# Optimization experiments

Hardware: AMD Instinct MI355X
Metric: run time of the kernel (lower is better)

## Reference

```python
import jax, jax.numpy as jnp
import numpy as np

H = 1024
NS, NQ, S = 32, 64, 256
ADAPT_STEPS = 5


def _mlp_ln(x, W1, b1, W2, b2, g, be):
    # Linear -> ReLU -> Linear -> LayerNorm (dropout is identity in eval)
    h = jax.nn.relu(x @ W1 + b1) @ W2 + b2
    mu = h.mean(-1, keepdims=True)
    var = ((h - mu) ** 2).mean(-1, keepdims=True)
    return g * (h - mu) / jnp.sqrt(var + 1e-5) + be


def setup_inputs() -> dict:
    key = jax.random.key(0)
    ks = jax.random.split(key, 16)
    d = {}
    d['support_embeddings'] = jax.random.normal(ks[0], (NS, S, H), jnp.float32)
    d['query_embeddings'] = jax.random.normal(ks[1], (NQ, S, H), jnp.float32)
    d['support_labels'] = jax.random.randint(ks[2], (NS, S), 0, 3)
    w = lambda k, fi, fo: jax.random.normal(k, (fi, fo), jnp.float32) * (1.0 / np.sqrt(fi))
    # aspect_aware encoder
    d['aw_W1'] = w(ks[3], H, H); d['aw_b1'] = jnp.zeros((H,), jnp.float32)
    d['aw_W2'] = w(ks[4], H, H); d['aw_b2'] = jnp.zeros((H,), jnp.float32)
    d['aw_g'] = jnp.ones((H,), jnp.float32); d['aw_be'] = jnp.zeros((H,), jnp.float32)
    # aspect_contrastive encoder
    d['ct_W1'] = w(ks[5], H, H); d['ct_b1'] = jnp.zeros((H,), jnp.float32)
    d['ct_W2'] = w(ks[6], H, H); d['ct_b2'] = jnp.zeros((H,), jnp.float32)
    d['ct_g'] = jnp.ones((H,), jnp.float32); d['ct_be'] = jnp.zeros((H,), jnp.float32)
    # adaptation net (randomly-initialized 2-layer MLP in the torch code)
    d['ad_W1'] = w(ks[7], H, H); d['ad_b1'] = jnp.zeros((H,), jnp.float32)
    d['ad_W2'] = w(ks[8], H, H); d['ad_b2'] = jnp.zeros((H,), jnp.float32)
    # meta classifier
    d['cl_W1'] = w(ks[9], 2 * H, H); d['cl_b1'] = jnp.zeros((H,), jnp.float32)
    d['cl_W2'] = w(ks[10], H, 64); d['cl_b2'] = jnp.zeros((64,), jnp.float32)
    d['cl_W3'] = w(ks[11], 64, 3); d['cl_b3'] = jnp.zeros((3,), jnp.float32)
    return d


def reference(support_embeddings, query_embeddings, support_labels,
              aw_W1, aw_b1, aw_W2, aw_b2, aw_g, aw_be,
              ct_W1, ct_b1, ct_W2, ct_b2, ct_g, ct_be,
              ad_W1, ad_b1, ad_W2, ad_b2,
              cl_W1, cl_b1, cl_W2, cl_b2, cl_W3, cl_b3):
    # --- encode support set, build per-sentence aspect prototypes ---
    aw_s = _mlp_ln(support_embeddings, aw_W1, aw_b1, aw_W2, aw_b2, aw_g, aw_be)  # [NS,S,H]
    mask = (support_labels > 0).astype(aw_s.dtype)[..., None]                    # [NS,S,1]
    cnt = jnp.maximum(mask.sum(axis=1), 1.0)                                     # [NS,1]
    protos = (aw_s * mask).sum(axis=1) / cnt                                     # [NS,H] masked mean
    pn = protos / jnp.maximum(jnp.linalg.norm(protos, axis=-1, keepdims=True), 1e-8)

    # --- meta-adaptation: fused over all (query, token) pairs, 5 steps ---
    adapted = query_embeddings
    for _ in range(ADAPT_STEPS):
        qn = adapted / jnp.maximum(jnp.linalg.norm(adapted, axis=-1, keepdims=True), 1e-8)
        sims = jnp.einsum('qsh,ph->qsp', qn, pn)           # cosine similarities
        wts = jax.nn.softmax(sims, axis=-1)
        infl = jnp.einsum('qsp,ph->qsh', wts, protos)      # prototype influence
        adapted = jax.nn.relu((adapted + infl) @ ad_W1 + ad_b1) @ ad_W2 + ad_b2

    # --- classify adapted query tokens ---
    q_aw = _mlp_ln(adapted, aw_W1, aw_b1, aw_W2, aw_b2, aw_g, aw_be)
    q_ct = _mlp_ln(adapted, ct_W1, ct_b1, ct_W2, ct_b2, ct_g, ct_be)
    comb = jnp.concatenate([q_aw, q_ct], axis=-1)          # [NQ,S,2H]
    h = jax.nn.relu(comb @ cl_W1 + cl_b1)
    h = jax.nn.relu(h @ cl_W2 + cl_b2)
    preds = h @ cl_W3 + cl_b3                              # [NQ,S,3]
    return preds
```

## Files before the change

### kernel.cpp

```cpp
#include <hip/hip_runtime.h>
#include <hip/hip_bf16.h>

#define H 1024
#define NS 32
#define SS 256
#define T_Q 16384
#define M_S 8192

typedef __hip_bfloat16 bf16;
typedef short short8 __attribute__((ext_vector_type(8)));
typedef float floatx4 __attribute__((ext_vector_type(4)));

__device__ __forceinline__ float ldf(const bf16& v) { return __bfloat162float(v); }

__device__ __forceinline__ void split2(float v, bf16& h, bf16& l) {
  h = __float2bfloat16(v);
  l = __float2bfloat16(v - __bfloat162float(h));
}

__device__ __forceinline__ void gl2lds16(const void* g, void* l) {
  __builtin_amdgcn_global_load_lds(
      (const __attribute__((address_space(1))) unsigned int*)g,
      (__attribute__((address_space(3))) unsigned int*)l, 16, 0, 0);
}

__device__ __forceinline__ short8 ld8s(const bf16* p) { return *(const short8*)p; }

__global__ __launch_bounds__(256) void conv_split(const float* __restrict__ in,
                                                  bf16* __restrict__ oh,
                                                  bf16* __restrict__ ol, int n)
{
  int i = blockIdx.x * 256 + threadIdx.x;
  if (i < n) { bf16 h, l; split2(in[i], h, l); oh[i] = h; ol[i] = l; }
}

__global__ __launch_bounds__(256) void transpose_split(
    const float* __restrict__ W, bf16* __restrict__ Wh, bf16* __restrict__ Wl,
    int K, int N)
{
  __shared__ float t[32][33];
  int n0 = blockIdx.x * 32, k0 = blockIdx.y * 32;
  int tx = threadIdx.x & 31, ty = threadIdx.x >> 5;
#pragma unroll
  for (int i = 0; i < 32; i += 8)
    t[ty + i][tx] = W[(size_t)(k0 + ty + i) * N + (n0 + tx)];
  __syncthreads();
#pragma unroll
  for (int i = 0; i < 32; i += 8) {
    bf16 h, l; split2(t[tx][ty + i], h, l);
    size_t o = (size_t)(n0 + ty + i) * K + (k0 + tx);
    Wh[o] = h;
    if (Wl) Wl[o] = l;
  }
}

template<bool RELU, bool HASWL>
__global__ __launch_bounds__(512) void gemm3p(
    const bf16* __restrict__ A0h, const bf16* __restrict__ A0l,
    const bf16* __restrict__ A1h, const bf16* __restrict__ A1l,
    const bf16* __restrict__ Wh,  const bf16* __restrict__ Wl,
    const float* __restrict__ bias,
    bf16* __restrict__ Ch, bf16* __restrict__ Cl,
    int M, int N, int K0, int Ktot)
{
  (void)M;
  __shared__ __align__(16) bf16 lds[3 * 24576];
  const int tid = threadIdx.x;
  const int w = tid >> 6, l = tid & 63;
  const int bm0 = blockIdx.x * 256, bn0 = blockIdx.y * 128;
  const int wr = w >> 1, wn = w & 1;
  const int m16 = l & 15, quad = l >> 4;
  const int srow = l & 15;
  const int scol = (l >> 4) * 8;

  floatx4 acc[4][4];
#pragma unroll
  for (int i = 0; i < 4; i++)
#pragma unroll
    for (int j = 0; j < 4; j++) { acc[i][j][0]=0.f; acc[i][j][1]=0.f; acc[i][j][2]=0.f; acc[i][j][3]=0.f; }

  const size_t raA0 = (size_t)(bm0 + (2 * w)     * 16 + srow) * H + scol;
  const size_t raA1 = (size_t)(bm0 + (2 * w + 1) * 16 + srow) * H + scol;
  const size_t raB  = (size_t)(bn0 + w * 16 + srow) * Ktot + scol;
  const int nT = Ktot >> 5;

  auto stage = [&](int t) {
    const int k0 = t << 5;
    const bf16 *Abh, *Abl; int ke;
    if (k0 < K0) { Abh = A0h; Abl = A0l; ke = k0; }
    else         { Abh = A1h; Abl = A1l; ke = k0 - K0; }
    bf16* buf = lds + (t % 3) * 24576;
    gl2lds16(Abh + raA0 + ke, buf + (2 * w)     * 512);
    gl2lds16(Abh + raA1 + ke, buf + (2 * w + 1) * 512);
    gl2lds16(Abl + raA0 + ke, buf + 8192 + (2 * w)     * 512);
    gl2lds16(Abl + raA1 + ke, buf + 8192 + (2 * w + 1) * 512);
    gl2lds16(Wh + raB + k0, buf + 16384 + w * 512);
    if (HASWL) gl2lds16(Wl + raB + k0, buf + 20480 + w * 512);
  };

  stage(0);
  if (nT > 1) stage(1);

  const int la = l * 8;
  for (int t = 0; t < nT; ++t) {
    const bf16* buf = lds + (t % 3) * 24576;
    if (t + 2 < nT) {
      stage(t + 2);
      if (HASWL) asm volatile("s_waitcnt vmcnt(12)" ::: "memory");
      else       asm volatile("s_waitcnt vmcnt(10)" ::: "memory");
    } else if (t + 1 < nT) {
      if (HASWL) asm volatile("s_waitcnt vmcnt(6)" ::: "memory");
      else       asm volatile("s_waitcnt vmcnt(5)" ::: "memory");
    } else {
      asm volatile("s_waitcnt vmcnt(0)" ::: "memory");
    }
    __builtin_amdgcn_s_barrier();

    const bf16* bA  = buf + (wr * 4) * 512 + la;
    const bf16* bAl = bA + 8192;
    const bf16* bB  = buf + 16384 + (wn * 4) * 512 + la;
    const bf16* bBl = bB + 4096;

    short8 bh[4], bl8[4];
#pragma unroll
    for (int ni = 0; ni < 4; ni++) bh[ni] = ld8s(bB + ni * 512);
    if (HASWL) {
#pragma unroll
      for (int ni = 0; ni < 4; ni++) bl8[ni] = ld8s(bBl + ni * 512);
    }

#define MM3(MI, AH, AL)                                                                            \
    _Pragma("unroll")                                                                              \
    for (int ni = 0; ni < 4; ni++) {                                                               \
      acc[MI][ni] = __builtin_amdgcn_mfma_f32_16x16x32_bf16(AH, bh[ni],  acc[MI][ni], 0, 0, 0);    \
      acc[MI][ni] = __builtin_amdgcn_mfma_f32_16x16x32_bf16(AL, bh[ni],  acc[MI][ni], 0, 0, 0);    \
      if (HASWL)                                                                                   \
        acc[MI][ni] = __builtin_amdgcn_mfma_f32_16x16x32_bf16(AH, bl8[ni], acc[MI][ni], 0, 0, 0);  \
    }

    {
      short8 a0h = ld8s(bA),          a1h = ld8s(bA + 512);
      short8 a0l = ld8s(bAl),         a1l = ld8s(bAl + 512);
      __builtin_amdgcn_s_setprio(1);
      MM3(0, a0h, a0l)
      MM3(1, a1h, a1l)
      __builtin_amdgcn_s_setprio(0);
    }
    __builtin_amdgcn_s_barrier();
    {
      short8 a2h = ld8s(bA + 1024),   a3h = ld8s(bA + 1536);
      short8 a2l = ld8s(bAl + 1024),  a3l = ld8s(bAl + 1536);
      __builtin_amdgcn_s_setprio(1);
      MM3(2, a2h, a2l)
      MM3(3, a3h, a3l)
      __builtin_amdgcn_s_setprio(0);
    }
    __builtin_amdgcn_s_barrier();
#undef MM3
  }

#pragma unroll
  for (int mi = 0; mi < 4; mi++) {
#pragma unroll
    for (int ni = 0; ni < 4; ni++) {
      int row0 = bm0 + wr * 64 + mi * 16 + quad * 4;
      int col  = bn0 + wn * 64 + ni * 16 + m16;
      float bv = bias ? bias[col] : 0.f;
#pragma unroll
      for (int r = 0; r < 4; r++) {
        float v = acc[mi][ni][r] + bv;
        if (RELU) v = fmaxf(v, 0.f);
        bf16 h, lo; split2(v, h, lo);
        size_t o = (size_t)(row0 + r) * N + col;
        Ch[o] = h; Cl[o] = lo;
      }
    }
  }
}

__global__ __launch_bounds__(256) void ln_pair(
    bf16* __restrict__ hh, bf16* __restrict__ hl,
    const float* __restrict__ g, const float* __restrict__ be)
{
  int row = blockIdx.x;
  bf16* ph = hh + (size_t)row * H;
  bf16* pl = hl + (size_t)row * H;
  int tid = threadIdx.x;
  float v[4];
  float s = 0.f, sq = 0.f;
#pragma unroll
  for (int j = 0; j < 4; j++) {
    int hi = tid + 256 * j;
    v[j] = ldf(ph[hi]) + ldf(pl[hi]);
    s += v[j]; sq += v[j] * v[j];
  }
  __shared__ float rs[256], rq[256];
  rs[tid] = s; rq[tid] = sq; __syncthreads();
  for (int o = 128; o; o >>= 1) {
    if (tid < o) { rs[tid] += rs[tid + o]; rq[tid] += rq[tid + o]; }
    __syncthreads();
  }
  float mu   = rs[0] * (1.0f / H);
  float var  = rq[0] * (1.0f / H) - mu * mu;
  float rstd = rsqrtf(var + 1e-5f);
#pragma unroll
  for (int j = 0; j < 4; j++) {
    int hi = tid + 256 * j;
    bf16 h, l; split2(g[hi] * (v[j] - mu) * rstd + be[hi], h, l);
    ph[hi] = h; pl[hi] = l;
  }
}

__global__ __launch_bounds__(256) void proto_kernel(
    const bf16* __restrict__ eh, const bf16* __restrict__ el,
    const int* __restrict__ labels, float* __restrict__ protos_out)
{
  int p = blockIdx.x;
  int tid = threadIdx.x;
  __shared__ unsigned char lbl[SS];
  lbl[tid] = (labels[p * SS + tid] > 0) ? 1 : 0;
  __syncthreads();
  float acc[4] = {0.f, 0.f, 0.f, 0.f};
  int cnt = 0;
  const bf16* bh = eh + (size_t)p * SS * H;
  const bf16* bl = el + (size_t)p * SS * H;
  for (int s = 0; s < SS; s++) {
    if (lbl[s]) {
      cnt++;
      const bf16* rh = bh + (size_t)s * H;
      const bf16* rl = bl + (size_t)s * H;
#pragma unroll
      for (int j = 0; j < 4; j++)
        acc[j] += ldf(rh[tid + 256 * j]) + ldf(rl[tid + 256 * j]);
    }
  }
  float ic = 1.0f / fmaxf((float)cnt, 1.0f);
#pragma unroll
  for (int j = 0; j < 4; j++) protos_out[p * H + tid + 256 * j] = acc[j] * ic;
}

__global__ __launch_bounds__(256) void pn_kernel(
    const float* __restrict__ protos, bf16* __restrict__ pnh, bf16* __restrict__ pnl)
{
  int p = blockIdx.x;
  int tid = threadIdx.x;
  __shared__ float red[256];
  float v[4];
  float sq = 0.f;
#pragma unroll
  for (int j = 0; j < 4; j++) { v[j] = protos[p * H + tid + 256 * j]; sq += v[j] * v[j]; }
  red[tid] = sq; __syncthreads();
  for (int o = 128; o; o >>= 1) {
    if (tid < o) red[tid] += red[tid + o];
    __syncthreads();
  }
  float inv = 1.0f / fmaxf(sqrtf(red[0]), 1e-8f);
#pragma unroll
  for (int j = 0; j < 4; j++) {
    bf16 h, l; split2(v[j] * inv, h, l);
    pnh[p * H + tid + 256 * j] = h;
    pnl[p * H + tid + 256 * j] = l;
  }
}

__global__ __launch_bounds__(256) void rownorm_pair(
    const bf16* __restrict__ hh, const bf16* __restrict__ hl, float* __restrict__ rn)
{
  int row = blockIdx.x;
  int tid = threadIdx.x;
  const bf16* ph = hh + (size_t)row * H;
  const bf16* pl = hl + (size_t)row * H;
  float s = 0.f;
#pragma unroll
  for (int j = 0; j < 4; j++) {
    float v = ldf(ph[tid + 256 * j]) + ldf(pl[tid + 256 * j]);
    s += v * v;
  }
  __shared__ float rs[256];
  rs[tid] = s; __syncthreads();
  for (int o = 128; o; o >>= 1) {
    if (tid < o) rs[tid] += rs[tid + o];
    __syncthreads();
  }
  if (tid == 0) rn[row] = 1.0f / fmaxf(sqrtf(rs[0]), 1e-8f);
}

__global__ __launch_bounds__(256) void sims_mfma(
    const bf16* __restrict__ Ah, const bf16* __restrict__ Al,
    const bf16* __restrict__ Bh, const bf16* __restrict__ Bl,
    float* __restrict__ sims)
{
  __shared__ bf16 AsH[64 * 32];
  __shared__ bf16 AsL[64 * 32];
  __shared__ bf16 BsH[32 * 32];
  __shared__ bf16 BsL[32 * 32];
  const int tid = threadIdx.x;
  const int w = tid >> 6, l = tid & 63;
  const int bm0 = blockIdx.x * 64;
  const int m16 = l & 15, quad = l >> 4;
  const int sr = l >> 2;
  const int sc = (l & 3) * 8;

  floatx4 acc[2];
#pragma unroll
  for (int nt = 0; nt < 2; nt++) { acc[nt][0]=0.f; acc[nt][1]=0.f; acc[nt][2]=0.f; acc[nt][3]=0.f; }

  for (int k0 = 0; k0 < H; k0 += 32) {
    gl2lds16(Ah + (size_t)(bm0 + w * 16 + sr) * H + k0 + sc, &AsH[w * 512]);
    gl2lds16(Al + (size_t)(bm0 + w * 16 + sr) * H + k0 + sc, &AsL[w * 512]);
    if (w < 2) gl2lds16(Bh + (size_t)(w * 16 + sr) * H + k0 + sc, &BsH[w * 512]);
    else       gl2lds16(Bl + (size_t)((w - 2) * 16 + sr) * H + k0 + sc, &BsL[(w - 2) * 512]);
    __syncthreads();

    short8 ah  = *(const short8*)&AsH[(w * 16 + m16) * 32 + quad * 8];
    short8 al8 = *(const short8*)&AsL[(w * 16 + m16) * 32 + quad * 8];
#pragma unroll
    for (int nt = 0; nt < 2; nt++) {
      short8 bh  = *(const short8*)&BsH[(nt * 16 + m16) * 32 + quad * 8];
      short8 bl8 = *(const short8*)&BsL[(nt * 16 + m16) * 32 + quad * 8];
      acc[nt] = __builtin_amdgcn_mfma_f32_16x16x32_bf16(ah,  bh,  acc[nt], 0, 0, 0);
      acc[nt] = __builtin_amdgcn_mfma_f32_16x16x32_bf16(al8, bh,  acc[nt], 0, 0, 0);
      acc[nt] = __builtin_amdgcn_mfma_f32_16x16x32_bf16(ah,  bl8, acc[nt], 0, 0, 0);
    }
    __syncthreads();
  }

#pragma unroll
  for (int nt = 0; nt < 2; nt++) {
    int col  = nt * 16 + m16;
    int row0 = bm0 + w * 16 + quad * 4;
#pragma unroll
    for (int r = 0; r < 4; r++)
      sims[(size_t)(row0 + r) * 32 + col] = acc[nt][r];
  }
}

__global__ __launch_bounds__(256) void softmax32(
    const float* __restrict__ sims, const float* __restrict__ rn,
    float* __restrict__ wts)
{
  int t = blockIdx.x * 8 + (threadIdx.x >> 5);
  int p = threadIdx.x & 31;
  float s = sims[(size_t)t * 32 + p] * rn[t];
  float m = s;
#pragma unroll
  for (int o = 16; o; o >>= 1) m = fmaxf(m, __shfl_xor(m, o, 64));
  float e = __expf(s - m);
  float sum = e;
#pragma unroll
  for (int o = 16; o; o >>= 1) sum += __shfl_xor(sum, o, 64);
  wts[(size_t)t * 32 + p] = e / sum;
}

__global__ __launch_bounds__(256) void infl16(
    const bf16* __restrict__ ah, const bf16* __restrict__ al,
    const float* __restrict__ wts, const float* __restrict__ protos,
    bf16* __restrict__ oh, bf16* __restrict__ ol)
{
  int t0 = blockIdx.x * 16;
  int tid = threadIdx.x;
  __shared__ float wl[16][32];
  for (int i = tid; i < 512; i += 256)
    wl[i >> 5][i & 31] = wts[(size_t)(t0 + (i >> 5)) * 32 + (i & 31)];
  __syncthreads();
  int c0 = tid * 4;
  float acc[16][4];
#pragma unroll
  for (int tk = 0; tk < 16; tk++) {
    const bf16* rh = ah + (size_t)(t0 + tk) * H + c0;
    const bf16* rl = al + (size_t)(t0 + tk) * H + c0;
#pragma unroll
    for (int j = 0; j < 4; j++) acc[tk][j] = ldf(rh[j]) + ldf(rl[j]);
  }
  for (int p = 0; p < 32; p++) {
    float4 pv = *(const float4*)&protos[p * H + c0];
#pragma unroll
    for (int tk = 0; tk < 16; tk++) {
      float w = wl[tk][p];
      acc[tk][0] += w * pv.x; acc[tk][1] += w * pv.y;
      acc[tk][2] += w * pv.z; acc[tk][3] += w * pv.w;
    }
  }
#pragma unroll
  for (int tk = 0; tk < 16; tk++) {
    bf16* wh = oh + (size_t)(t0 + tk) * H + c0;
    bf16* wo = ol + (size_t)(t0 + tk) * H + c0;
#pragma unroll
    for (int j = 0; j < 4; j++) { bf16 h, lo; split2(acc[tk][j], h, lo); wh[j] = h; wo[j] = lo; }
  }
}

__global__ __launch_bounds__(256) void gemm_small(
    const bf16* __restrict__ Ah, const bf16* __restrict__ Al,
    const float* __restrict__ W, const float* __restrict__ bias,
    float* __restrict__ C, int M, int N, int K)
{
  const int BK = 16;
  __shared__ float As[BK][64];
  __shared__ float Bs[BK][64];
  int tid = threadIdx.x;
  int tx = tid & 15, ty = tid >> 4;
  int bn0 = blockIdx.x * 64;
  int bm0 = blockIdx.y * 64;
  float acc[4][4] = {};
  int am = tid >> 2, ak = (tid & 3) * 4;
  int bk = tid >> 4, bn = (tid & 15) * 4;
  const bf16* Aph = Ah + (size_t)(bm0 + am) * K + ak;
  const bf16* Apl = Al + (size_t)(bm0 + am) * K + ak;
  const float* Wptr = W + (size_t)bk * N + bn0 + bn;
  for (int k0 = 0; k0 < K; k0 += BK) {
#pragma unroll
    for (int c = 0; c < 4; c++) As[ak + c][am] = ldf(Aph[c]) + ldf(Apl[c]);
#pragma unroll
    for (int c = 0; c < 4; c++) Bs[bk][bn + c] = Wptr[c];
    __syncthreads();
#pragma unroll
    for (int k = 0; k < BK; k++) {
      float a[4], b[4];
#pragma unroll
      for (int i = 0; i < 4; i++) a[i] = As[k][ty * 4 + i];
#pragma unroll
      for (int j = 0; j < 4; j++) b[j] = Bs[k][tx * 4 + j];
#pragma unroll
      for (int i = 0; i < 4; i++)
#pragma unroll
        for (int j = 0; j < 4; j++)
          acc[i][j] += a[i] * b[j];
    }
    __syncthreads();
    Aph += BK; Apl += BK;
    Wptr += (size_t)BK * N;
  }
#pragma unroll
  for (int i = 0; i < 4; i++) {
    float* Crow = C + (size_t)(bm0 + ty * 4 + i) * N + bn0;
#pragma unroll
    for (int j = 0; j < 4; j++) {
      int n = tx * 4 + j;
      Crow[n] = fmaxf(acc[i][j] + bias[bn0 + n], 0.f);
    }
  }
}

__global__ __launch_bounds__(256) void FewShotABSALearner_46935402610855_kernel(
    const float* __restrict__ h2, const float* __restrict__ W3,
    const float* __restrict__ b3, float* __restrict__ out,
    int t0, int nElem, int out_size)
{
  int idx = blockIdx.x * 256 + threadIdx.x;
  if (idx >= nElem) return;
  int t = idx / 3, c = idx - t * 3;
  float acc = b3[c];
  const float* hr = h2 + (size_t)t * 64;
#pragma unroll
  for (int k = 0; k < 64; k++) acc += hr[k] * W3[k * 3 + c];
  int oi = t0 * 3 + idx;
  if (oi < out_size) out[oi] = acc;
}

extern "C" void kernel_launch(void* const* d_in, const int* in_sizes, int n_in,
                              void* d_out, int out_size, void* d_ws, size_t ws_size,
                              hipStream_t stream)
{
  (void)in_sizes; (void)n_in;
  const float* sup   = (const float*)d_in[0];
  const float* qry   = (const float*)d_in[1];
  const int*   lab   = (const int*)d_in[2];
  const float *aw_W1 = (const float*)d_in[3],  *aw_b1 = (const float*)d_in[4];
  const float *aw_W2 = (const float*)d_in[5],  *aw_b2 = (const float*)d_in[6];
  const float *aw_g  = (const float*)d_in[7],  *aw_be = (const float*)d_in[8];
  const float *ct_W1 = (const float*)d_in[9],  *ct_b1 = (const float*)d_in[10];
  const float *ct_W2 = (const float*)d_in[11], *ct_b2 = (const float*)d_in[12];
  const float *ct_g  = (const float*)d_in[13], *ct_be = (const float*)d_in[14];
  const float *ad_W1 = (const float*)d_in[15], *ad_b1 = (const float*)d_in[16];
  const float *ad_W2 = (const float*)d_in[17], *ad_b2 = (const float*)d_in[18];
  const float *cl_W1 = (const float*)d_in[19], *cl_b1 = (const float*)d_in[20];
  const float *cl_W2 = (const float*)d_in[21], *cl_b2 = (const float*)d_in[22];
  const float *cl_W3 = (const float*)d_in[23], *cl_b3 = (const float*)d_in[24];
  float* out = (float*)d_out;

  const size_t MB = 1 << 20;
  int C; bool clLo = true;
  if      (ws_size >= (size_t)239403008) C = 16384;
  else if (ws_size >= (size_t)136609792) C = 8192;
  else if (ws_size >= (size_t)85213184)  C = 4096;
  else if (ws_size >= (size_t)59514880)  C = 2048;
  else if (ws_size >= (size_t)46665728)  C = 1024;
  else { C = 1024; clLo = false; }
  const int Cs = (C < M_S) ? C : M_S;
  const size_t actB = (size_t)C * H * sizeof(bf16);

  char* ws = (char*)d_ws;
  size_t off = 0;
  auto nxt = [&](size_t b) { char* p = ws + off; off += b; return p; };
  bf16* sqw[12];
  for (int i = 0; i < 12; i++) sqw[i] = (bf16*)nxt(2 * MB);
  bf16 *aw1h = sqw[0], *aw1l = sqw[1], *aw2h = sqw[2],  *aw2l = sqw[3];
  bf16 *ct1h = sqw[4], *ct1l = sqw[5], *ct2h = sqw[6],  *ct2l = sqw[7];
  bf16 *ad1h = sqw[8], *ad1l = sqw[9], *ad2h = sqw[10], *ad2l = sqw[11];
  bf16* clW1h = (bf16*)nxt(4 * MB);
  bf16* clW1l = clLo ? (bf16*)nxt(4 * MB) : nullptr;
  float* protos = (float*)nxt(NS * H * 4);
  bf16*  pnh    = (bf16*)nxt(NS * H * 2);
  bf16*  pnl    = (bf16*)nxt(NS * H * 2);
  char*  ub     = nxt((size_t)C * 256);
  float* h2c   = (float*)ub;
  float* simsb = (float*)ub;
  float* wtsb  = (float*)(ub + (size_t)C * 128);
  float* rn    = (float*)nxt((size_t)C * 4);
  bf16 *R0h = (bf16*)nxt(actB), *R0l = (bf16*)nxt(actB);
  bf16 *R1h = (bf16*)nxt(actB), *R1l = (bf16*)nxt(actB);
  bf16 *R2h = (bf16*)nxt(actB), *R2l = (bf16*)nxt(actB);

  dim3 blk(256);
  dim3 blk2(512);
  dim3 tg(32, 32);
  dim3 gg2(C / 256, H / 128);
  dim3 gs2(Cs / 256, H / 128);

  transpose_split<<<tg, blk, 0, stream>>>(aw_W1, aw1h, aw1l, H, H);
  transpose_split<<<tg, blk, 0, stream>>>(aw_W2, aw2h, aw2l, H, H);
  transpose_split<<<tg, blk, 0, stream>>>(ct_W1, ct1h, ct1l, H, H);
  transpose_split<<<tg, blk, 0, stream>>>(ct_W2, ct2h, ct2l, H, H);
  transpose_split<<<tg, blk, 0, stream>>>(ad_W1, ad1h, ad1l, H, H);
  transpose_split<<<tg, blk, 0, stream>>>(ad_W2, ad2h, ad2l, H, H);
  transpose_split<<<dim3(32, 64), blk, 0, stream>>>(cl_W1, clW1h, clW1l, 2 * H, H);

  for (int sc = 0; sc < M_S / Cs; sc++) {
    conv_split<<<(Cs * H) / 256, blk, 0, stream>>>(sup + (size_t)sc * Cs * H, R0h, R0l, Cs * H);
    gemm3p<true , true><<<gs2, blk2, 0, stream>>>(R0h, R0l, R0h, R0l, aw1h, aw1l, aw_b1, R1h, R1l, Cs, H, H, H);
    gemm3p<false, true><<<gs2, blk2, 0, stream>>>(R1h, R1l, R1h, R1l, aw2h, aw2l, aw_b2, R2h, R2l, Cs, H, H, H);
    ln_pair<<<Cs, blk, 0, stream>>>(R2h, R2l, aw_g, aw_be);
    proto_kernel<<<Cs / SS, blk, 0, stream>>>(R2h, R2l, lab + sc * Cs,
                                              protos + (size_t)sc * (Cs / SS) * H);
  }
  pn_kernel<<<NS, blk, 0, stream>>>(protos, pnh, pnl);

  for (int qc = 0; qc < T_Q / C; qc++) {
    const float* q0 = qry + (size_t)qc * C * H;
    conv_split<<<(C * H) / 256, blk, 0, stream>>>(q0, R2h, R2l, C * H);
    for (int it = 0; it < 5; it++) {
      rownorm_pair<<<C, blk, 0, stream>>>(R2h, R2l, rn);
      sims_mfma<<<C / 64, blk, 0, stream>>>(R2h, R2l, pnh, pnl, simsb);
      softmax32<<<C / 8, blk, 0, stream>>>(simsb, rn, wtsb);
      infl16<<<C / 16, blk, 0, stream>>>(R2h, R2l, wtsb, protos, R0h, R0l);
      gemm3p<true , true><<<gg2, blk2, 0, stream>>>(R0h, R0l, R0h, R0l, ad1h, ad1l, ad_b1, R1h, R1l, C, H, H, H);
      gemm3p<false, true><<<gg2, blk2, 0, stream>>>(R1h, R1l, R1h, R1l, ad2h, ad2l, ad_b2, R2h, R2l, C, H, H, H);
    }
    gemm3p<true , true><<<gg2, blk2, 0, stream>>>(R2h, R2l, R2h, R2l, aw1h, aw1l, aw_b1, R0h, R0l, C, H, H, H);
    gemm3p<false, true><<<gg2, blk2, 0, stream>>>(R0h, R0l, R0h, R0l, aw2h, aw2l, aw_b2, R1h, R1l, C, H, H, H);
    ln_pair<<<C, blk, 0, stream>>>(R1h, R1l, aw_g, aw_be);
    gemm3p<true , true><<<gg2, blk2, 0, stream>>>(R2h, R2l, R2h, R2l, ct1h, ct1l, ct_b1, R0h, R0l, C, H, H, H);
    gemm3p<false, true><<<gg2, blk2, 0, stream>>>(R0h, R0l, R0h, R0l, ct2h, ct2l, ct_b2, R2h, R2l, C, H, H, H);
    ln_pair<<<C, blk, 0, stream>>>(R2h, R2l, ct_g, ct_be);
    if (clLo)
      gemm3p<true, true ><<<gg2, blk2, 0, stream>>>(R1h, R1l, R2h, R2l, clW1h, clW1l, cl_b1, R0h, R0l, C, H, H, 2 * H);
    else
      gemm3p<true, false><<<gg2, blk2, 0, stream>>>(R1h, R1l, R2h, R2l, clW1h, nullptr, cl_b1, R0h, R0l, C, H, H, 2 * H);
    gemm_small<<<dim3(1, C / 64), blk, 0, stream>>>(R0h, R0l, cl_W2, cl_b2, h2c, C, 64, H);
    FewShotABSALearner_46935402610855_kernel<<<(C * 3 + 255) / 256, blk, 0, stream>>>(
        h2c, cl_W3, cl_b3, out, qc * C, C * 3, out_size);
  }
}
```

Before: 2.740 ms.

## Enlarge GEMM tile to 256x256 with XCD-aware block mapping and double buffering

The split-bf16 GEMM now computes a 256x256 output tile per 512-thread block instead of 256x128. Each wave holds an 8x4 accumulator grid and A fragments are software-prefetched across the m-loop. The LDS pipeline drops from triple to double buffering, and the 2D grid becomes a 1D grid remapped so blocks on the same XCD share a B column tile. The intent is more arithmetic per loaded byte and better L2 locality. The cost is more accumulator registers, less prefetch depth and fewer blocks, which may hurt occupancy and latency hiding.

```diff
diff --git a/kernel.cpp b/kernel.cpp
--- a/kernel.cpp
+++ b/kernel.cpp
@@ -55,7 +55,7 @@
 }
 
 template<bool RELU, bool HASWL>
-__global__ __launch_bounds__(512) void gemm3p(
+__global__ __launch_bounds__(512, 2) void gemm3p(
     const bf16* __restrict__ A0h, const bf16* __restrict__ A0l,
     const bf16* __restrict__ A1h, const bf16* __restrict__ A1l,
     const bf16* __restrict__ Wh,  const bf16* __restrict__ Wl,
@@ -64,24 +64,30 @@
     int M, int N, int K0, int Ktot)
 {
   (void)M;
-  __shared__ __align__(16) bf16 lds[3 * 24576];
+  __shared__ __align__(16) bf16 lds[2 * 32768];
   const int tid = threadIdx.x;
   const int w = tid >> 6, l = tid & 63;
-  const int bm0 = blockIdx.x * 256, bn0 = blockIdx.y * 128;
-  const int wr = w >> 1, wn = w & 1;
+  const int nbm = gridDim.x >> 2;
+  const int lid = blockIdx.x;
+  const int xcd = lid & 7, ib = lid >> 3;
+  const int half = nbm >> 1;
+  const int bn = xcd >> 1;
+  const int bm = (xcd & 1) * half + ib;
+  const int wr = w >> 2, wn = w & 3;
   const int m16 = l & 15, quad = l >> 4;
   const int srow = l & 15;
   const int scol = (l >> 4) * 8;
 
-  floatx4 acc[4][4];
-#pragma unroll
-  for (int i = 0; i < 4; i++)
+  floatx4 acc[8][4];
+#pragma unroll
+  for (int i = 0; i < 8; i++)
 #pragma unroll
     for (int j = 0; j < 4; j++) { acc[i][j][0]=0.f; acc[i][j][1]=0.f; acc[i][j][2]=0.f; acc[i][j][3]=0.f; }
 
-  const size_t raA0 = (size_t)(bm0 + (2 * w)     * 16 + srow) * H + scol;
-  const size_t raA1 = (size_t)(bm0 + (2 * w + 1) * 16 + srow) * H + scol;
-  const size_t raB  = (size_t)(bn0 + w * 16 + srow) * Ktot + scol;
+  const size_t raA0 = (size_t)(bm * 256 + (2 * w)     * 16 + srow) * H + scol;
+  const size_t raA1 = (size_t)(bm * 256 + (2 * w + 1) * 16 + srow) * H + scol;
+  const size_t raB0 = (size_t)(bn * 256 + (2 * w)     * 16 + srow) * Ktot + scol;
+  const size_t raB1 = (size_t)(bn * 256 + (2 * w + 1) * 16 + srow) * Ktot + scol;
   const int nT = Ktot >> 5;
 
   auto stage = [&](int t) {
@@ -89,86 +95,75 @@
     const bf16 *Abh, *Abl; int ke;
     if (k0 < K0) { Abh = A0h; Abl = A0l; ke = k0; }
     else         { Abh = A1h; Abl = A1l; ke = k0 - K0; }
-    bf16* buf = lds + (t % 3) * 24576;
+    bf16* buf = lds + (t & 1) * 32768;
     gl2lds16(Abh + raA0 + ke, buf + (2 * w)     * 512);
     gl2lds16(Abh + raA1 + ke, buf + (2 * w + 1) * 512);
-    gl2lds16(Abl + raA0 + ke, buf + 8192 + (2 * w)     * 512);
-    gl2lds16(Abl + raA1 + ke, buf + 8192 + (2 * w + 1) * 512);
-    gl2lds16(Wh + raB + k0, buf + 16384 + w * 512);
-    if (HASWL) gl2lds16(Wl + raB + k0, buf + 20480 + w * 512);
+    gl2lds16(Abl + raA0 + ke, buf + 8192  + (2 * w)     * 512);
+    gl2lds16(Abl + raA1 + ke, buf + 8192  + (2 * w + 1) * 512);
+    gl2lds16(Wh + raB0 + k0, buf + 16384 + (2 * w)     * 512);
+    gl2lds16(Wh + raB1 + k0, buf + 16384 + (2 * w + 1) * 512);
+    if (HASWL) {
+      gl2lds16(Wl + raB0 + k0, buf + 24576 + (2 * w)     * 512);
+      gl2lds16(Wl + raB1 + k0, buf + 24576 + (2 * w + 1) * 512);
+    }
   };
 
   stage(0);
-  if (nT > 1) stage(1);
 
   const int la = l * 8;
   for (int t = 0; t < nT; ++t) {
-    const bf16* buf = lds + (t % 3) * 24576;
-    if (t + 2 < nT) {
-      stage(t + 2);
-      if (HASWL) asm volatile("s_waitcnt vmcnt(12)" ::: "memory");
-      else       asm volatile("s_waitcnt vmcnt(10)" ::: "memory");
-    } else if (t + 1 < nT) {
-      if (HASWL) asm volatile("s_waitcnt vmcnt(6)" ::: "memory");
-      else       asm volatile("s_waitcnt vmcnt(5)" ::: "memory");
+    const bf16* buf = lds + (t & 1) * 32768;
+    __builtin_amdgcn_s_barrier();
+    if (t + 1 < nT) {
+      stage(t + 1);
+      if (HASWL) asm volatile("s_waitcnt vmcnt(8)" ::: "memory");
+      else       asm volatile("s_waitcnt vmcnt(6)" ::: "memory");
     } else {
       asm volatile("s_waitcnt vmcnt(0)" ::: "memory");
     }
     __builtin_amdgcn_s_barrier();
 
-    const bf16* bA  = buf + (wr * 4) * 512 + la;
-    const bf16* bAl = bA + 8192;
-    const bf16* bB  = buf + 16384 + (wn * 4) * 512 + la;
-    const bf16* bBl = bB + 4096;
+    const bf16* pA  = buf + (wr * 8) * 512 + la;
+    const bf16* pAl = pA + 8192;
+    const bf16* pB  = buf + 16384 + (wn * 4) * 512 + la;
+    const bf16* pBl = pB + 8192;
 
     short8 bh[4], bl8[4];
 #pragma unroll
-    for (int ni = 0; ni < 4; ni++) bh[ni] = ld8s(bB + ni * 512);
+    for (int nt = 0; nt < 4; nt++) bh[nt] = ld8s(pB + nt * 512);
     if (HASWL) {
 #pragma unroll
-      for (int ni = 0; ni < 4; ni++) bl8[ni] = ld8s(bBl + ni * 512);
-    }
-
-#define MM3(MI, AH, AL)                                                                            \
-    _Pragma("unroll")                                                                              \
-    for (int ni = 0; ni < 4; ni++) {                                                               \
-      acc[MI][ni] = __builtin_amdgcn_mfma_f32_16x16x32_bf16(AH, bh[ni],  acc[MI][ni], 0, 0, 0);    \
-      acc[MI][ni] = __builtin_amdgcn_mfma_f32_16x16x32_bf16(AL, bh[ni],  acc[MI][ni], 0, 0, 0);    \
-      if (HASWL)                                                                                   \
-        acc[MI][ni] = __builtin_amdgcn_mfma_f32_16x16x32_bf16(AH, bl8[ni], acc[MI][ni], 0, 0, 0);  \
-    }
-
-    {
-      short8 a0h = ld8s(bA),          a1h = ld8s(bA + 512);
-      short8 a0l = ld8s(bAl),         a1l = ld8s(bAl + 512);
+      for (int nt = 0; nt < 4; nt++) bl8[nt] = ld8s(pBl + nt * 512);
+    }
+
+    short8 ah = ld8s(pA), al8 = ld8s(pAl);
+#pragma unroll
+    for (int mt = 0; mt < 8; mt++) {
+      short8 nh = ah, nl = al8;
+      if (mt < 7) { nh = ld8s(pA + (mt + 1) * 512); nl = ld8s(pAl + (mt + 1) * 512); }
       __builtin_amdgcn_s_setprio(1);
-      MM3(0, a0h, a0l)
-      MM3(1, a1h, a1l)
+#pragma unroll
+      for (int nt = 0; nt < 4; nt++) {
+        acc[mt][nt] = __builtin_amdgcn_mfma_f32_16x16x32_bf16(ah,  bh[nt],  acc[mt][nt], 0, 0, 0);
+        acc[mt][nt] = __builtin_amdgcn_mfma_f32_16x16x32_bf16(al8, bh[nt],  acc[mt][nt], 0, 0, 0);
+        if (HASWL)
+          acc[mt][nt] = __builtin_amdgcn_mfma_f32_16x16x32_bf16(ah, bl8[nt], acc[mt][nt], 0, 0, 0);
+      }
       __builtin_amdgcn_s_setprio(0);
-    }
-    __builtin_amdgcn_s_barrier();
-    {
-      short8 a2h = ld8s(bA + 1024),   a3h = ld8s(bA + 1536);
-      short8 a2l = ld8s(bAl + 1024),  a3l = ld8s(bAl + 1536);
-      __builtin_amdgcn_s_setprio(1);
-      MM3(2, a2h, a2l)
-      MM3(3, a3h, a3l)
-      __builtin_amdgcn_s_setprio(0);
-    }
-    __builtin_amdgcn_s_barrier();
-#undef MM3
-  }
-
-#pragma unroll
-  for (int mi = 0; mi < 4; mi++) {
-#pragma unroll
-    for (int ni = 0; ni < 4; ni++) {
-      int row0 = bm0 + wr * 64 + mi * 16 + quad * 4;
-      int col  = bn0 + wn * 64 + ni * 16 + m16;
+      ah = nh; al8 = nl;
+    }
+  }
+
+#pragma unroll
+  for (int mt = 0; mt < 8; mt++) {
+#pragma unroll
+    for (int nt = 0; nt < 4; nt++) {
+      int row0 = bm * 256 + wr * 128 + mt * 16 + quad * 4;
+      int col  = bn * 256 + wn * 64 + nt * 16 + m16;
       float bv = bias ? bias[col] : 0.f;
 #pragma unroll
       for (int r = 0; r < 4; r++) {
-        float v = acc[mi][ni][r] + bv;
+        float v = acc[mt][nt][r] + bv;
         if (RELU) v = fmaxf(v, 0.f);
         bf16 h, lo; split2(v, h, lo);
         size_t o = (size_t)(row0 + r) * N + col;
@@ -515,8 +510,8 @@
   dim3 blk(256);
   dim3 blk2(512);
   dim3 tg(32, 32);
-  dim3 gg2(C / 256, H / 128);
-  dim3 gs2(Cs / 256, H / 128);
+  dim3 ggq((C / 256) * 4);
+  dim3 ggs((Cs / 256) * 4);
 
   transpose_split<<<tg, blk, 0, stream>>>(aw_W1, aw1h, aw1l, H, H);
   transpose_split<<<tg, blk, 0, stream>>>(aw_W2, aw2h, aw2l, H, H);
@@ -528,8 +523,8 @@
 
   for (int sc = 0; sc < M_S / Cs; sc++) {
     conv_split<<<(Cs * H) / 256, blk, 0, stream>>>(sup + (size_t)sc * Cs * H, R0h, R0l, Cs * H);
-    gemm3p<true , true><<<gs2, blk2, 0, stream>>>(R0h, R0l, R0h, R0l, aw1h, aw1l, aw_b1, R1h, R1l, Cs, H, H, H);
-    gemm3p<false, true><<<gs2, blk2, 0, stream>>>(R1h, R1l, R1h, R1l, aw2h, aw2l, aw_b2, R2h, R2l, Cs, H, H, H);
+    gemm3p<true , true><<<ggs, blk2, 0, stream>>>(R0h, R0l, R0h, R0l, aw1h, aw1l, aw_b1, R1h, R1l, Cs, H, H, H);
+    gemm3p<false, true><<<ggs, blk2, 0, stream>>>(R1h, R1l, R1h, R1l, aw2h, aw2l, aw_b2, R2h, R2l, Cs, H, H, H);
     ln_pair<<<Cs, blk, 0, stream>>>(R2h, R2l, aw_g, aw_be);
     proto_kernel<<<Cs / SS, blk, 0, stream>>>(R2h, R2l, lab + sc * Cs,
                                               protos + (size_t)sc * (Cs / SS) * H);
@@ -544,19 +539,19 @@
       sims_mfma<<<C / 64, blk, 0, stream>>>(R2h, R2l, pnh, pnl, simsb);
       softmax32<<<C / 8, blk, 0, stream>>>(simsb, rn, wtsb);
       infl16<<<C / 16, blk, 0, stream>>>(R2h, R2l, wtsb, protos, R0h, R0l);
-      gemm3p<true , true><<<gg2, blk2, 0, stream>>>(R0h, R0l, R0h, R0l, ad1h, ad1l, ad_b1, R1h, R1l, C, H, H, H);
-      gemm3p<false, true><<<gg2, blk2, 0, stream>>>(R1h, R1l, R1h, R1l, ad2h, ad2l, ad_b2, R2h, R2l, C, H, H, H);
-    }
-    gemm3p<true , true><<<gg2, blk2, 0, stream>>>(R2h, R2l, R2h, R2l, aw1h, aw1l, aw_b1, R0h, R0l, C, H, H, H);
-    gemm3p<false, true><<<gg2, blk2, 0, stream>>>(R0h, R0l, R0h, R0l, aw2h, aw2l, aw_b2, R1h, R1l, C, H, H, H);
+      gemm3p<true , true><<<ggq, blk2, 0, stream>>>(R0h, R0l, R0h, R0l, ad1h, ad1l, ad_b1, R1h, R1l, C, H, H, H);
+      gemm3p<false, true><<<ggq, blk2, 0, stream>>>(R1h, R1l, R1h, R1l, ad2h, ad2l, ad_b2, R2h, R2l, C, H, H, H);
+    }
+    gemm3p<true , true><<<ggq, blk2, 0, stream>>>(R2h, R2l, R2h, R2l, aw1h, aw1l, aw_b1, R0h, R0l, C, H, H, H);
+    gemm3p<false, true><<<ggq, blk2, 0, stream>>>(R0h, R0l, R0h, R0l, aw2h, aw2l, aw_b2, R1h, R1l, C, H, H, H);
     ln_pair<<<C, blk, 0, stream>>>(R1h, R1l, aw_g, aw_be);
-    gemm3p<true , true><<<gg2, blk2, 0, stream>>>(R2h, R2l, R2h, R2l, ct1h, ct1l, ct_b1, R0h, R0l, C, H, H, H);
-    gemm3p<false, true><<<gg2, blk2, 0, stream>>>(R0h, R0l, R0h, R0l, ct2h, ct2l, ct_b2, R2h, R2l, C, H, H, H);
+    gemm3p<true , true><<<ggq, blk2, 0, stream>>>(R2h, R2l, R2h, R2l, ct1h, ct1l, ct_b1, R0h, R0l, C, H, H, H);
+    gemm3p<false, true><<<ggq, blk2, 0, stream>>>(R0h, R0l, R0h, R0l, ct2h, ct2l, ct_b2, R2h, R2l, C, H, H, H);
     ln_pair<<<C, blk, 0, stream>>>(R2h, R2l, ct_g, ct_be);
     if (clLo)
-      gemm3p<true, true ><<<gg2, blk2, 0, stream>>>(R1h, R1l, R2h, R2l, clW1h, clW1l, cl_b1, R0h, R0l, C, H, H, 2 * H);
+      gemm3p<true, true ><<<ggq, blk2, 0, stream>>>(R1h, R1l, R2h, R2l, clW1h, clW1l, cl_b1, R0h, R0l, C, H, H, 2 * H);
     else
-      gemm3p<true, false><<<gg2, blk2, 0, stream>>>(R1h, R1l, R2h, R2l, clW1h, nullptr, cl_b1, R0h, R0l, C, H, H, 2 * H);
+      gemm3p<true, false><<<ggq, blk2, 0, stream>>>(R1h, R1l, R2h, R2l, clW1h, nullptr, cl_b1, R0h, R0l, C, H, H, 2 * H);
     gemm_small<<<dim3(1, C / 64), blk, 0, stream>>>(R0h, R0l, cl_W2, cl_b2, h2c, C, 64, H);
     FewShotABSALearner_46935402610855_kernel<<<(C * 3 + 255) / 256, blk, 0, stream>>>(
         h2c, cl_W3, cl_b3, out, qc * C, C * 3, out_size);
```

Result: faster. 2.629 ms (-4.1%).
